# Kernel tuning notes

Hardware: AMD Instinct MI355X
Metric: run time of the kernel (lower is better)

The kernel has to match this reference:

```python
import jax, jax.numpy as jnp
import numpy as np

D = 1024
H = 16
DH = D // H
MAX_TYPES = 256
B, L = 8, 1024
EPS = 1e-5


def setup_inputs() -> dict:
    key = jax.random.key(0)
    ks = jax.random.split(key, 16)
    s = 0.02
    return {
        'type_ids': jax.random.randint(ks[0], (B, L), 0, MAX_TYPES),
        'values': jax.random.normal(ks[1], (B, L, 1), jnp.float32),
        'deltas': jax.random.uniform(ks[2], (B, L, 1), jnp.float32),
        'type_emb': jax.random.normal(ks[3], (MAX_TYPES, D), jnp.float32) * s,
        'Wv': jax.random.normal(ks[4], (D, 1), jnp.float32) * s,
        'bv': jnp.zeros((D,), jnp.float32),
        'Wt': jax.random.normal(ks[5], (D, 1), jnp.float32) * s,
        'bt': jnp.zeros((D,), jnp.float32),
        'Win': jax.random.normal(ks[6], (3 * D, D), jnp.float32) * s,
        'bin': jnp.zeros((3 * D,), jnp.float32),
        'Wout': jax.random.normal(ks[7], (D, D), jnp.float32) * s,
        'bout': jnp.zeros((D,), jnp.float32),
        'W1': jax.random.normal(ks[8], (D, D), jnp.float32) * s,
        'b1': jnp.zeros((D,), jnp.float32),
        'W2': jax.random.normal(ks[9], (D, D), jnp.float32) * s,
        'b2': jnp.zeros((D,), jnp.float32),
        'gamma': jnp.ones((D,), jnp.float32),
        'beta': jnp.zeros((D,), jnp.float32),
    }


def _ln(x, gamma, beta):
    mu = jnp.mean(x, axis=-1, keepdims=True)
    var = jnp.mean(jnp.square(x - mu), axis=-1, keepdims=True)
    return (x - mu) * jax.lax.rsqrt(var + EPS) * gamma + beta


def reference(type_ids, values, deltas, type_emb, Wv, bv, Wt, bt,
              Win, bin, Wout, bout, W1, b1, W2, b2, gamma, beta):
    # fused embedding: type lookup + value/time linear projections
    h = type_emb[type_ids] + values @ Wv.T + bv + deltas @ Wt.T + bt  # [B,L,D]
    b, l, d = h.shape
    # multi-head self-attention (explicit weights path, need_weights=True)
    qkv = h @ Win.T + bin  # [B,L,3D]
    q, k, v = jnp.split(qkv, 3, axis=-1)
    q = q.reshape(b, l, H, DH)
    k = k.reshape(b, l, H, DH)
    v = v.reshape(b, l, H, DH)
    scale = 1.0 / jnp.sqrt(jnp.asarray(DH, h.dtype))
    scores = jnp.einsum('blhd,bmhd->bhlm', q, k) * scale  # [B,H,L,L]
    w = jax.nn.softmax(scores, axis=-1)
    attn = jnp.einsum('bhlm,bmhd->blhd', w, v).reshape(b, l, d)
    attn_out = attn @ Wout.T + bout
    h2 = _ln(h + attn_out, gamma, beta)
    ff = jax.nn.relu(h2 @ W1.T + b1) @ W2.T + b2
    h3 = _ln(h2 + ff, gamma, beta)
    pooled = h3.mean(axis=1)  # [B,D]
    attn_tokens = w.mean(axis=1).mean(axis=2)  # mean over heads, then keys -> [B,L]
    return pooled, attn_tokens
```

## Files before the change

kernel.cpp:

```cpp
#include <hip/hip_runtime.h>
#include <hip/hip_bf16.h>


#define Dm 1024
#define Hh 16
#define Bb 8
#define Ll 1024
#define Mm 8192
#define LNEPS 1e-5f

typedef __attribute__((ext_vector_type(8))) short s16x8;
typedef __attribute__((ext_vector_type(4))) short s16x4;
typedef __attribute__((ext_vector_type(4))) float f32x4;

using bf16 = __hip_bfloat16;

__device__ __forceinline__ short f2bs(float f) {
  return __builtin_bit_cast(short, __float2bfloat16(f));
}
__device__ __forceinline__ float b2f(short s) {
  return __builtin_bit_cast(float, ((unsigned)(unsigned short)s) << 16);
}

__device__ __forceinline__ unsigned cvtpk(float lo, float hi) {
  unsigned r;
  asm("v_cvt_pk_bf16_f32 %0, %1, %2" : "=v"(r) : "v"(lo), "v"(hi));
  return r;
}

__device__ __forceinline__ void gload16(const void* g, void* l) {
  __builtin_amdgcn_global_load_lds(
      (__attribute__((address_space(1))) void*)g,
      (__attribute__((address_space(3))) void*)l, 16, 0, 0);
}

__global__ __launch_bounds__(256) void k_f2b4(
    const float* __restrict__ w0, const float* __restrict__ w1,
    const float* __restrict__ w2, const float* __restrict__ w3,
    bf16* __restrict__ o0, bf16* __restrict__ o1,
    bf16* __restrict__ o2, bf16* __restrict__ o3)
{
  const int bId = blockIdx.x;
  const float* src; bf16* dst; int rel;
  if (bId < 3072)      { src = w0; dst = o0; rel = bId; }
  else if (bId < 4096) { src = w1; dst = o1; rel = bId - 3072; }
  else if (bId < 5120) { src = w2; dst = o2; rel = bId - 4096; }
  else                 { src = w3; dst = o3; rel = bId - 5120; }
  const size_t i = ((size_t)rel * 256 + threadIdx.x) * 4;
  const float4 v = *(const float4*)&src[i];
  s16x4 o;
  o[0] = f2bs(v.x); o[1] = f2bs(v.y); o[2] = f2bs(v.z); o[3] = f2bs(v.w);
  *(s16x4*)&dst[i] = o;
}

__global__ __launch_bounds__(256) void k_embed(
    const int* __restrict__ tids, const float* __restrict__ vals, const float* __restrict__ dels,
    const float* __restrict__ temb, const float* __restrict__ Wv, const float* __restrict__ bv,
    const float* __restrict__ Wt, const float* __restrict__ bt,
    bf16* __restrict__ hb)
{
  const int row = blockIdx.x;
  const int ty = tids[row];
  const float v = vals[row], dl = dels[row];
  const int d0 = threadIdx.x * 4;
  const float4 e  = *(const float4*)&temb[(size_t)ty * Dm + d0];
  const float4 wv = *(const float4*)&Wv[d0];
  const float4 c1 = *(const float4*)&bv[d0];
  const float4 wt = *(const float4*)&Wt[d0];
  const float4 c2 = *(const float4*)&bt[d0];
  s16x4 o;
  o[0] = f2bs(e.x + v * wv.x + c1.x + dl * wt.x + c2.x);
  o[1] = f2bs(e.y + v * wv.y + c1.y + dl * wt.y + c2.y);
  o[2] = f2bs(e.z + v * wv.z + c1.z + dl * wt.z + c2.z);
  o[3] = f2bs(e.w + v * wv.w + c1.w + dl * wt.w + c2.w);
  *(s16x4*)((short*)hb + (size_t)row * Dm + d0) = o;
}

template<bool RELU, bool RES>
__global__ __launch_bounds__(512) void k_gemm8(
    const bf16* __restrict__ A, const bf16* __restrict__ Bt,
    const float* __restrict__ bias, const bf16* __restrict__ res,
    bf16* __restrict__ outB, const int N, const int K)
{
  __shared__ __attribute__((aligned(16))) short lds[49152];
  const int tid = threadIdx.x, lane = tid & 63, wave = tid >> 6;
  const int wr = wave >> 2, wc = wave & 3;
  const int l15 = lane & 15, lg = (lane >> 4) & 3;
  const int bm = blockIdx.x, bn = blockIdx.y;
  const int NT = K >> 6;

  const int rl = tid >> 3;
  const int swz = ((tid & 7) ^ (rl & 7)) * 8;
  const bf16* aSrc = A  + (size_t)(bm * 128 + rl) * K + swz;
  const bf16* bSrc = Bt + (size_t)(bn * 256 + rl) * K + swz;

  f32x4 acc[4][4] = {};

  auto stageA = [&](int t, int h) {
    gload16(aSrc + (size_t)h * 64 * K + t * 64,
            &lds[(t & 1) * 24576 + h * 4096 + tid * 8]);
  };
  auto stageB = [&](int t, int h) {
    gload16(bSrc + (size_t)h * 128 * K + t * 64,
            &lds[(t & 1) * 24576 + 8192 + h * 8192 + tid * 8]);
    gload16(bSrc + (size_t)(h * 128 + 64) * K + t * 64,
            &lds[(t & 1) * 24576 + 8192 + h * 8192 + 4096 + tid * 8]);
  };

  stageA(0, 0); stageA(0, 1); stageB(0, 0); stageB(0, 1);
  if (NT > 1) { stageA(1, 0); stageA(1, 1); }
  asm volatile("s_waitcnt vmcnt(2)" ::: "memory");
  __builtin_amdgcn_sched_barrier(0);
  __builtin_amdgcn_s_barrier();

  for (int t = 0; t < NT; ++t) {
    const int cb = (t & 1) * 24576;
    s16x8 fa[4][2], fb[2][2];

#pragma unroll
    for (int m = 0; m < 4; ++m)
#pragma unroll
      for (int ks = 0; ks < 2; ++ks) {
        const int row = wr * 64 + m * 16 + l15;
        fa[m][ks] = *(const s16x8*)&lds[cb + row * 64 + (((ks * 4 + lg) ^ (row & 7)) << 3)];
      }
#pragma unroll
    for (int n = 0; n < 2; ++n)
#pragma unroll
      for (int ks = 0; ks < 2; ++ks) {
        const int row = wc * 64 + n * 16 + l15;
        fb[n][ks] = *(const s16x8*)&lds[cb + 8192 + row * 64 + (((ks * 4 + lg) ^ (row & 7)) << 3)];
      }
    if (t + 1 < NT) { stageB(t + 1, 0); stageB(t + 1, 1); }
    __builtin_amdgcn_s_barrier();
    asm volatile("s_waitcnt lgkmcnt(0)" ::: "memory");
    __builtin_amdgcn_sched_barrier(0);
    __builtin_amdgcn_s_setprio(1);
#pragma unroll
    for (int m = 0; m < 4; ++m)
#pragma unroll
      for (int n = 0; n < 2; ++n)
#pragma unroll
        for (int ks = 0; ks < 2; ++ks)
          acc[m][n] = __builtin_amdgcn_mfma_f32_16x16x32_bf16(fa[m][ks], fb[n][ks], acc[m][n], 0, 0, 0);
    __builtin_amdgcn_s_setprio(0);
    __builtin_amdgcn_s_barrier();

#pragma unroll
    for (int n = 0; n < 2; ++n)
#pragma unroll
      for (int ks = 0; ks < 2; ++ks) {
        const int row = wc * 64 + (2 + n) * 16 + l15;
        fb[n][ks] = *(const s16x8*)&lds[cb + 8192 + row * 64 + (((ks * 4 + lg) ^ (row & 7)) << 3)];
      }
    if (t + 2 < NT) { stageA(t + 2, 0); stageA(t + 2, 1); }
    __builtin_amdgcn_s_barrier();
    asm volatile("s_waitcnt lgkmcnt(0)" ::: "memory");
    __builtin_amdgcn_sched_barrier(0);
    __builtin_amdgcn_s_setprio(1);
#pragma unroll
    for (int m = 0; m < 4; ++m)
#pragma unroll
      for (int n = 0; n < 2; ++n)
#pragma unroll
        for (int ks = 0; ks < 2; ++ks)
          acc[m][2 + n] = __builtin_amdgcn_mfma_f32_16x16x32_bf16(fa[m][ks], fb[n][ks], acc[m][2 + n], 0, 0, 0);
    __builtin_amdgcn_s_setprio(0);

    if (t + 1 < NT) {
      if (t + 2 < NT) asm volatile("s_waitcnt vmcnt(2)" ::: "memory");
      else            asm volatile("s_waitcnt vmcnt(0)" ::: "memory");
      __builtin_amdgcn_sched_barrier(0);
      __builtin_amdgcn_s_barrier();
    }
  }

#pragma unroll
  for (int n = 0; n < 4; ++n) {
    const int col = bn * 256 + wc * 64 + n * 16 + l15;
    const float bc = bias[col];
#pragma unroll
    for (int m = 0; m < 4; ++m) {
#pragma unroll
      for (int i = 0; i < 4; ++i) {
        const size_t row = (size_t)bm * 128 + wr * 64 + m * 16 + lg * 4 + i;
        float v = acc[m][n][i] + bc;
        if constexpr (RES)  v += b2f(((const short*)res)[row * N + col]);
        if constexpr (RELU) v = fmaxf(v, 0.f);
        outB[row * N + col] = __float2bfloat16(v);
      }
    }
  }
}

__global__ __launch_bounds__(256) void k_vt(const bf16* __restrict__ qkv, bf16* __restrict__ vt)
{
  const int bh = blockIdx.x, lc = blockIdx.y;
  const int b = bh >> 4, h = bh & 15;
  __shared__ short tile[64][72];
  const int r = threadIdx.x >> 2;
  const int c0 = (threadIdx.x & 3) << 4;
  const short* src = (const short*)qkv + ((size_t)(b * Ll + lc * 64 + r)) * 3072 + 2048 + h * 64 + c0;
  const s16x8 x0 = *(const s16x8*)src;
  const s16x8 x1 = *(const s16x8*)(src + 8);
#pragma unroll
  for (int j = 0; j < 8; ++j) { tile[r][c0 + j] = x0[j]; tile[r][c0 + 8 + j] = x1[j]; }
  __syncthreads();
  s16x8 y0, y1;
#pragma unroll
  for (int j = 0; j < 8; ++j) { y0[j] = tile[c0 + j][r]; y1[j] = tile[c0 + 8 + j][r]; }
  short* dst = (short*)vt + ((size_t)(bh * 64 + r)) * Ll + lc * 64 + c0;
  *(s16x8*)dst = y0;
  *(s16x8*)(dst + 8) = y1;
}

__global__ __launch_bounds__(256) void k_attn(
    const bf16* __restrict__ qkv, const bf16* __restrict__ vt, bf16* __restrict__ attnb)
{
  const int bh = blockIdx.x;
  const int qb = blockIdx.y;
  const int b = bh >> 4, h = bh & 15;
  __shared__ __attribute__((aligned(16))) short lK[8192];
  __shared__ __attribute__((aligned(16))) short lV[8192];
  __shared__ __attribute__((aligned(16))) short lP[8192];
  const int tid = threadIdx.x, lane = tid & 63, wave = tid >> 6;
  const int l15 = lane & 15, lg = lane >> 4;
  const int qrow = wave * 32;
  const int l7 = l15 & 7;

  s16x8 qf[2][2];
#pragma unroll
  for (int mq = 0; mq < 2; ++mq)
#pragma unroll
    for (int ks = 0; ks < 2; ++ks)
      qf[mq][ks] = *(const s16x8*)((const short*)qkv +
          ((size_t)(b * Ll + qb * 128 + qrow + mq * 16 + l15)) * 3072 + h * 64 + ks * 32 + lg * 8);

  f32x4 o[2][4] = {};
  float rs[2] = {0.f, 0.f};

  const int sr = tid >> 3;
  const int swz = (tid & 7) ^ (sr & 7);

  auto stage = [&](int mc) {
    const int bo = (mc & 1) * 4096;
    const bf16* gk = qkv + ((size_t)(b * Ll + mc * 64 + sr)) * 3072 + 1024 + h * 64 + swz * 8;
    gload16(gk,                     &lK[bo + tid * 8]);
    gload16(gk + (size_t)32 * 3072, &lK[bo + 2048 + tid * 8]);
    const bf16* gv = vt + ((size_t)(bh * 64 + sr)) * Ll + mc * 64 + swz * 8;
    gload16(gv,                   &lV[bo + tid * 8]);
    gload16(gv + (size_t)32 * Ll, &lV[bo + 2048 + tid * 8]);
  };

  stage(0);

  for (int mc = 0; mc < 16; ++mc) {
    asm volatile("s_waitcnt vmcnt(0)" ::: "memory");
    __builtin_amdgcn_s_barrier();
    __builtin_amdgcn_sched_barrier(0);
    if (mc + 1 < 16) stage(mc + 1);
    const int bo = (mc & 1) * 4096;

    f32x4 st[2][4] = {};
    __builtin_amdgcn_s_setprio(1);
#pragma unroll
    for (int ks = 0; ks < 2; ++ks) {
#pragma unroll
      for (int n = 0; n < 4; ++n) {
        const int kr = n * 16 + l15;
        const s16x8 kf = *(const s16x8*)&lK[bo + kr * 64 + (((ks * 4 + lg) ^ l7) << 3)];
        st[0][n] = __builtin_amdgcn_mfma_f32_16x16x32_bf16(kf, qf[0][ks], st[0][n], 0, 0, 0);
        st[1][n] = __builtin_amdgcn_mfma_f32_16x16x32_bf16(kf, qf[1][ks], st[1][n], 0, 0, 0);
      }
    }
    __builtin_amdgcn_s_setprio(0);

#pragma unroll
    for (int mq = 0; mq < 2; ++mq) {
      const int qr = qrow + mq * 16 + l15;
      short* prow = &lP[qr * 64];
      float loc = 0.f;
#pragma unroll
      for (int n = 0; n < 4; ++n) {
        const float e0 = __expf(st[mq][n][0] * 0.125f);
        const float e1 = __expf(st[mq][n][1] * 0.125f);
        const float e2 = __expf(st[mq][n][2] * 0.125f);
        const float e3 = __expf(st[mq][n][3] * 0.125f);
        loc += (e0 + e1) + (e2 + e3);
        const unsigned c0 = cvtpk(e0, e1);
        const unsigned c1 = cvtpk(e2, e3);
        const int col0 = n * 16 + lg * 4;
        const int scol = ((((col0 >> 3) ^ (qr & 7)) << 3) | (col0 & 7));
        *(unsigned*)&prow[scol]     = c0;
        *(unsigned*)&prow[scol + 2] = c1;
      }
      rs[mq] += loc;
    }

    __builtin_amdgcn_s_setprio(1);
#pragma unroll
    for (int ks = 0; ks < 2; ++ks) {
      s16x8 pa[2];
#pragma unroll
      for (int mq = 0; mq < 2; ++mq) {
        const int qr = qrow + mq * 16 + l15;
        pa[mq] = *(const s16x8*)&lP[qr * 64 + (((ks * 4 + lg) ^ (qr & 7)) << 3)];
      }
#pragma unroll
      for (int dn = 0; dn < 4; ++dn) {
        const int vr = dn * 16 + l15;
        const s16x8 vf = *(const s16x8*)&lV[bo + vr * 64 + (((ks * 4 + lg) ^ l7) << 3)];
        o[0][dn] = __builtin_amdgcn_mfma_f32_16x16x32_bf16(pa[0], vf, o[0][dn], 0, 0, 0);
        o[1][dn] = __builtin_amdgcn_mfma_f32_16x16x32_bf16(pa[1], vf, o[1][dn], 0, 0, 0);
      }
    }
    __builtin_amdgcn_s_setprio(0);
    asm volatile("s_waitcnt lgkmcnt(0)" ::: "memory");
  }

#pragma unroll
  for (int mq = 0; mq < 2; ++mq) {
    rs[mq] += __shfl_xor(rs[mq], 16);
    rs[mq] += __shfl_xor(rs[mq], 32);
  }
#pragma unroll
  for (int mq = 0; mq < 2; ++mq) {
    float inv[4];
#pragma unroll
    for (int i = 0; i < 4; ++i)
      inv[i] = 1.f / __shfl(rs[mq], lg * 4 + i);
#pragma unroll
    for (int dn = 0; dn < 4; ++dn) {
#pragma unroll
      for (int i = 0; i < 4; ++i) {
        const int q = qb * 128 + qrow + mq * 16 + lg * 4 + i;
        attnb[((size_t)(b * Ll + q)) * Dm + h * 64 + dn * 16 + l15] =
            __float2bfloat16(o[mq][dn][i] * inv[i]);
      }
    }
  }
}

__global__ __launch_bounds__(256) void k_ln(const bf16* __restrict__ x,
    const float* __restrict__ gamma, const float* __restrict__ beta,
    bf16* __restrict__ y)
{
  const size_t row = blockIdx.x;
  const int d0 = threadIdx.x * 4;
  const s16x4 xv = *(const s16x4*)((const short*)x + row * Dm + d0);
  float f0 = b2f(xv[0]), f1 = b2f(xv[1]), f2 = b2f(xv[2]), f3 = b2f(xv[3]);
  float s  = (f0 + f1) + (f2 + f3);
  float ss = (f0 * f0 + f1 * f1) + (f2 * f2 + f3 * f3);
#pragma unroll
  for (int m = 1; m < 64; m <<= 1) { s += __shfl_xor(s, m); ss += __shfl_xor(ss, m); }
  __shared__ float red[8];
  const int wv = threadIdx.x >> 6;
  if ((threadIdx.x & 63) == 0) { red[wv] = s; red[4 + wv] = ss; }
  __syncthreads();
  s  = red[0] + red[1] + red[2] + red[3];
  ss = red[4] + red[5] + red[6] + red[7];
  const float mu = s * (1.f / Dm);
  const float rstd = rsqrtf(ss * (1.f / Dm) - mu * mu + LNEPS);
  const float4 g  = *(const float4*)&gamma[d0];
  const float4 be = *(const float4*)&beta[d0];
  s16x4 o;
  o[0] = f2bs((f0 - mu) * rstd * g.x + be.x);
  o[1] = f2bs((f1 - mu) * rstd * g.y + be.y);
  o[2] = f2bs((f2 - mu) * rstd * g.z + be.z);
  o[3] = f2bs((f3 - mu) * rstd * g.w + be.w);
  *(s16x4*)((short*)y + row * Dm + d0) = o;
}

__global__ __launch_bounds__(256) void k_pool_part(const bf16* __restrict__ h3, float* __restrict__ part)
{
  const int b = blockIdx.x, lcn = blockIdx.y, dz = blockIdx.z;
  const int d = dz * 256 + threadIdx.x;
  float s = 0.f;
#pragma unroll 4
  for (int l = 0; l < 64; ++l)
    s += b2f(((const short*)h3)[((size_t)(b * Ll + lcn * 64 + l)) * Dm + d]);
  part[((size_t)(b * 16 + lcn)) * Dm + d] = s;
}

__global__ __launch_bounds__(256) void k_pool_fin(const float* __restrict__ part, float* __restrict__ out)
{
  const int b = blockIdx.x;
  const int d = blockIdx.y * 256 + threadIdx.x;
  float s = 0.f;
#pragma unroll
  for (int c = 0; c < 16; ++c) s += part[((size_t)(b * 16 + c)) * Dm + d];
  out[b * Dm + d] = s * (1.f / Ll);
  out[(size_t)Mm + b * Dm + d] = 1.f / Ll;
}

extern "C" void kernel_launch(void* const* d_in, const int* in_sizes, int n_in,
                              void* d_out, int out_size, void* d_ws, size_t ws_size,
                              hipStream_t stream) {
  const int*   tids  = (const int*)  d_in[0];
  const float* vals  = (const float*)d_in[1];
  const float* dels  = (const float*)d_in[2];
  const float* temb  = (const float*)d_in[3];
  const float* Wv    = (const float*)d_in[4];
  const float* bv    = (const float*)d_in[5];
  const float* Wt    = (const float*)d_in[6];
  const float* bt    = (const float*)d_in[7];
  const float* Win   = (const float*)d_in[8];
  const float* bin   = (const float*)d_in[9];
  const float* Wout  = (const float*)d_in[10];
  const float* bout  = (const float*)d_in[11];
  const float* W1    = (const float*)d_in[12];
  const float* b1    = (const float*)d_in[13];
  const float* W2    = (const float*)d_in[14];
  const float* b2    = (const float*)d_in[15];
  const float* gamma = (const float*)d_in[16];
  const float* beta  = (const float*)d_in[17];
  float* out = (float*)d_out;

  char* w = (char*)d_ws;
  const size_t MB = 1ull << 20;
  bf16*  hb    = (bf16*) (w + 0);
  bf16*  qkv   = (bf16*) (w + 16 * MB);
  bf16*  vtb   = (bf16*) (w + 64 * MB);
  bf16*  attnb = (bf16*) (w + 80 * MB);
  bf16*  x1b   = (bf16*) (w + 16 * MB);
  bf16*  h2b   = (bf16*) (w + 32 * MB);
  bf16*  ff1   = (bf16*) (w + 48 * MB);
  bf16*  x2b   = (bf16*) (w + 64 * MB);
  bf16*  h3b   = (bf16*) (w + 80 * MB);
  bf16*  WinB  = (bf16*) (w + 96 * MB);
  bf16*  WoutB = (bf16*) (w + 102 * MB);
  bf16*  W1B   = (bf16*) (w + 104 * MB);
  bf16*  W2B   = (bf16*) (w + 106 * MB);
  float* part  = (float*)(w + 108 * MB);

  k_f2b4<<<6144, 256, 0, stream>>>(Win, Wout, W1, W2, WinB, WoutB, W1B, W2B);

  k_embed<<<Mm, 256, 0, stream>>>(tids, vals, dels, temb, Wv, bv, Wt, bt, hb);

  k_gemm8<false, false><<<dim3(64, 12), 512, 0, stream>>>(
      hb, WinB, bin, nullptr, qkv, 3072, 1024);

  k_vt<<<dim3(128, 16), 256, 0, stream>>>(qkv, vtb);
  k_attn<<<dim3(128, 8), 256, 0, stream>>>(qkv, vtb, attnb);

  k_gemm8<false, true><<<dim3(64, 4), 512, 0, stream>>>(
      attnb, WoutB, bout, hb, x1b, 1024, 1024);

  k_ln<<<Mm, 256, 0, stream>>>(x1b, gamma, beta, h2b);

  k_gemm8<true, false><<<dim3(64, 4), 512, 0, stream>>>(
      h2b, W1B, b1, nullptr, ff1, 1024, 1024);

  k_gemm8<false, true><<<dim3(64, 4), 512, 0, stream>>>(
      ff1, W2B, b2, h2b, x2b, 1024, 1024);

  k_ln<<<Mm, 256, 0, stream>>>(x2b, gamma, beta, h3b);

  k_pool_part<<<dim3(8, 16, 4), 256, 0, stream>>>(h3b, part);
  k_pool_fin<<<dim3(8, 4), 256, 0, stream>>>(part, out);
}
```

Measured before the change: 242.7 us.

## Use 32x32x16 MFMA in attention and keep P in registers via permlane swap

Rewrites the attention inner loop to use 32x32x16 bf16 MFMAs instead of 16x16x32, and transposes the QK^T accumulator layout in registers with v_permlane32_swap so P feeds the PV MFMA directly. This removes the LDS staging buffer for P, its swizzled stores and reloads, and the trailing lgkmcnt wait. It also switches exp to exp2f with a folded log2e scale. The cost is higher register pressure from the 16-wide accumulators and more complex lane mapping in the normalisation epilogue.

Result: no change. 247.4 us (+1.9%).

```diff
diff --git a/kernel.cpp b/kernel.cpp
--- a/kernel.cpp
+++ b/kernel.cpp
@@ -12,6 +12,7 @@
 typedef __attribute__((ext_vector_type(8))) short s16x8;
 typedef __attribute__((ext_vector_type(4))) short s16x4;
 typedef __attribute__((ext_vector_type(4))) float f32x4;
+typedef __attribute__((ext_vector_type(16))) float f32x16;
 
 using bf16 = __hip_bfloat16;
 
@@ -26,6 +27,9 @@
   unsigned r;
   asm("v_cvt_pk_bf16_f32 %0, %1, %2" : "=v"(r) : "v"(lo), "v"(hi));
   return r;
+}
+__device__ __forceinline__ void perm32(unsigned &a, unsigned &b) {
+  asm volatile("v_permlane32_swap_b32 %0, %1" : "+v"(a), "+v"(b));
 }
 
 __device__ __forceinline__ void gload16(const void* g, void* l) {
@@ -217,27 +221,25 @@
 __global__ __launch_bounds__(256) void k_attn(
     const bf16* __restrict__ qkv, const bf16* __restrict__ vt, bf16* __restrict__ attnb)
 {
-  const int bh = blockIdx.x;
-  const int qb = blockIdx.y;
+  const int bh = blockIdx.x, qb = blockIdx.y;
   const int b = bh >> 4, h = bh & 15;
   __shared__ __attribute__((aligned(16))) short lK[8192];
   __shared__ __attribute__((aligned(16))) short lV[8192];
-  __shared__ __attribute__((aligned(16))) short lP[8192];
   const int tid = threadIdx.x, lane = tid & 63, wave = tid >> 6;
-  const int l15 = lane & 15, lg = lane >> 4;
+  const int l31 = lane & 31, hi = lane >> 5;
+  const int r7 = l31 & 7;
   const int qrow = wave * 32;
-  const int l7 = l15 & 7;
-
-  s16x8 qf[2][2];
-#pragma unroll
-  for (int mq = 0; mq < 2; ++mq)
-#pragma unroll
-    for (int ks = 0; ks < 2; ++ks)
-      qf[mq][ks] = *(const s16x8*)((const short*)qkv +
-          ((size_t)(b * Ll + qb * 128 + qrow + mq * 16 + l15)) * 3072 + h * 64 + ks * 32 + lg * 8);
-
-  f32x4 o[2][4] = {};
-  float rs[2] = {0.f, 0.f};
+
+  s16x8 qf[4];
+  {
+    const short* qp = (const short*)qkv +
+        ((size_t)(b * Ll + qb * 128 + qrow + l31)) * 3072 + h * 64 + hi * 8;
+#pragma unroll
+    for (int s = 0; s < 4; ++s) qf[s] = *(const s16x8*)(qp + s * 16);
+  }
+
+  f32x16 o[2] = {};
+  float rsa[4] = {0.f, 0.f, 0.f, 0.f};
 
   const int sr = tid >> 3;
   const int swz = (tid & 7) ^ (sr & 7);
@@ -245,11 +247,11 @@
   auto stage = [&](int mc) {
     const int bo = (mc & 1) * 4096;
     const bf16* gk = qkv + ((size_t)(b * Ll + mc * 64 + sr)) * 3072 + 1024 + h * 64 + swz * 8;
-    gload16(gk,                     &lK[bo + tid * 8]);
-    gload16(gk + (size_t)32 * 3072, &lK[bo + 2048 + tid * 8]);
+    gload16(gk,                      &lK[bo + tid * 8]);
+    gload16(gk + (size_t)32 * 3072,  &lK[bo + 2048 + tid * 8]);
     const bf16* gv = vt + ((size_t)(bh * 64 + sr)) * Ll + mc * 64 + swz * 8;
-    gload16(gv,                   &lV[bo + tid * 8]);
-    gload16(gv + (size_t)32 * Ll, &lV[bo + 2048 + tid * 8]);
+    gload16(gv,                    &lV[bo + tid * 8]);
+    gload16(gv + (size_t)32 * Ll,  &lV[bo + 2048 + tid * 8]);
   };
 
   stage(0);
@@ -261,82 +263,59 @@
     if (mc + 1 < 16) stage(mc + 1);
     const int bo = (mc & 1) * 4096;
 
-    f32x4 st[2][4] = {};
+    f32x16 st[2] = {};
     __builtin_amdgcn_s_setprio(1);
 #pragma unroll
-    for (int ks = 0; ks < 2; ++ks) {
-#pragma unroll
-      for (int n = 0; n < 4; ++n) {
-        const int kr = n * 16 + l15;
-        const s16x8 kf = *(const s16x8*)&lK[bo + kr * 64 + (((ks * 4 + lg) ^ l7) << 3)];
-        st[0][n] = __builtin_amdgcn_mfma_f32_16x16x32_bf16(kf, qf[0][ks], st[0][n], 0, 0, 0);
-        st[1][n] = __builtin_amdgcn_mfma_f32_16x16x32_bf16(kf, qf[1][ks], st[1][n], 0, 0, 0);
-      }
+    for (int s = 0; s < 4; ++s) {
+      const int sl = ((2 * s + hi) ^ r7) << 3;
+      const s16x8 kf0 = *(const s16x8*)&lK[bo + l31 * 64 + sl];
+      const s16x8 kf1 = *(const s16x8*)&lK[bo + (32 + l31) * 64 + sl];
+      st[0] = __builtin_amdgcn_mfma_f32_32x32x16_bf16(kf0, qf[s], st[0], 0, 0, 0);
+      st[1] = __builtin_amdgcn_mfma_f32_32x32x16_bf16(kf1, qf[s], st[1], 0, 0, 0);
     }
     __builtin_amdgcn_s_setprio(0);
 
 #pragma unroll
-    for (int mq = 0; mq < 2; ++mq) {
-      const int qr = qrow + mq * 16 + l15;
-      short* prow = &lP[qr * 64];
-      float loc = 0.f;
-#pragma unroll
-      for (int n = 0; n < 4; ++n) {
-        const float e0 = __expf(st[mq][n][0] * 0.125f);
-        const float e1 = __expf(st[mq][n][1] * 0.125f);
-        const float e2 = __expf(st[mq][n][2] * 0.125f);
-        const float e3 = __expf(st[mq][n][3] * 0.125f);
-        loc += (e0 + e1) + (e2 + e3);
-        const unsigned c0 = cvtpk(e0, e1);
-        const unsigned c1 = cvtpk(e2, e3);
-        const int col0 = n * 16 + lg * 4;
-        const int scol = ((((col0 >> 3) ^ (qr & 7)) << 3) | (col0 & 7));
-        *(unsigned*)&prow[scol]     = c0;
-        *(unsigned*)&prow[scol + 2] = c1;
-      }
-      rs[mq] += loc;
+    for (int t = 0; t < 2; ++t) {
+#pragma unroll
+      for (int r = 0; r < 16; ++r) {
+        const float e = exp2f(st[t][r] * 0.18033688f);
+        rsa[r & 3] += e;
+        st[t][r] = e;
+      }
+#pragma unroll
+      for (int g = 0; g < 2; ++g) {
+        unsigned c0 = cvtpk(st[t][8 * g + 0], st[t][8 * g + 1]);
+        unsigned c1 = cvtpk(st[t][8 * g + 2], st[t][8 * g + 3]);
+        unsigned c2 = cvtpk(st[t][8 * g + 4], st[t][8 * g + 5]);
+        unsigned c3 = cvtpk(st[t][8 * g + 6], st[t][8 * g + 7]);
+        perm32(c0, c2);
+        perm32(c1, c3);
+        uint4 wda; wda.x = c0; wda.y = c1; wda.z = c2; wda.w = c3;
+        const s16x8 pa = __builtin_bit_cast(s16x8, wda);
+        const int s = 2 * t + g;
+        const int sl = ((2 * s + hi) ^ r7) << 3;
+        const s16x8 vf0 = *(const s16x8*)&lV[bo + l31 * 64 + sl];
+        const s16x8 vf1 = *(const s16x8*)&lV[bo + (32 + l31) * 64 + sl];
+        o[0] = __builtin_amdgcn_mfma_f32_32x32x16_bf16(pa, vf0, o[0], 0, 0, 0);
+        o[1] = __builtin_amdgcn_mfma_f32_32x32x16_bf16(pa, vf1, o[1], 0, 0, 0);
+      }
     }
-
-    __builtin_amdgcn_s_setprio(1);
-#pragma unroll
-    for (int ks = 0; ks < 2; ++ks) {
-      s16x8 pa[2];
-#pragma unroll
-      for (int mq = 0; mq < 2; ++mq) {
-        const int qr = qrow + mq * 16 + l15;
-        pa[mq] = *(const s16x8*)&lP[qr * 64 + (((ks * 4 + lg) ^ (qr & 7)) << 3)];
-      }
-#pragma unroll
-      for (int dn = 0; dn < 4; ++dn) {
-        const int vr = dn * 16 + l15;
-        const s16x8 vf = *(const s16x8*)&lV[bo + vr * 64 + (((ks * 4 + lg) ^ l7) << 3)];
-        o[0][dn] = __builtin_amdgcn_mfma_f32_16x16x32_bf16(pa[0], vf, o[0][dn], 0, 0, 0);
-        o[1][dn] = __builtin_amdgcn_mfma_f32_16x16x32_bf16(pa[1], vf, o[1][dn], 0, 0, 0);
-      }
-    }
-    __builtin_amdgcn_s_setprio(0);
-    asm volatile("s_waitcnt lgkmcnt(0)" ::: "memory");
   }
 
-#pragma unroll
-  for (int mq = 0; mq < 2; ++mq) {
-    rs[mq] += __shfl_xor(rs[mq], 16);
-    rs[mq] += __shfl_xor(rs[mq], 32);
-  }
-#pragma unroll
-  for (int mq = 0; mq < 2; ++mq) {
-    float inv[4];
-#pragma unroll
-    for (int i = 0; i < 4; ++i)
-      inv[i] = 1.f / __shfl(rs[mq], lg * 4 + i);
-#pragma unroll
-    for (int dn = 0; dn < 4; ++dn) {
-#pragma unroll
-      for (int i = 0; i < 4; ++i) {
-        const int q = qb * 128 + qrow + mq * 16 + lg * 4 + i;
-        attnb[((size_t)(b * Ll + q)) * Dm + h * 64 + dn * 16 + l15] =
-            __float2bfloat16(o[mq][dn][i] * inv[i]);
-      }
+  float rs = (rsa[0] + rsa[1]) + (rsa[2] + rsa[3]);
+  rs += __shfl_xor(rs, 32);
+  float inv[16];
+#pragma unroll
+  for (int r = 0; r < 16; ++r)
+    inv[r] = 1.f / __shfl(rs, (r & 3) + 8 * (r >> 2) + 4 * hi);
+#pragma unroll
+  for (int t = 0; t < 2; ++t) {
+#pragma unroll
+    for (int r = 0; r < 16; ++r) {
+      const int q = qb * 128 + qrow + (r & 3) + 8 * (r >> 2) + 4 * hi;
+      attnb[((size_t)(b * Ll + q)) * Dm + h * 64 + t * 32 + l31] =
+          __float2bfloat16(o[t][r] * inv[r]);
     }
   }
 }
```

## Fuse V transpose into QKV GEMM epilogue, fold softmax scale into Wq

Applied to the files above, without the earlier changes.

Merges weight conversion and embedding into a single prep kernel. The QKV GEMM epilogue now writes V directly in transposed per-head layout, replacing the separate transpose kernel. The softmax scale times log2(e) is folded into the Q weights and bias so attention can use exp2 without a multiply. This removes two launches and one pass over V, at the cost of strided, less coalesced 8-byte stores in the GEMM epilogue.

New measurement: 230.0 us, median of 2. -5.3%, faster.

```diff
diff --git a/kernel.cpp b/kernel.cpp
--- a/kernel.cpp
+++ b/kernel.cpp
@@ -8,6 +8,7 @@
 #define Ll 1024
 #define Mm 8192
 #define LNEPS 1e-5f
+#define QSCALE 0.18033688f
 
 typedef __attribute__((ext_vector_type(8))) short s16x8;
 typedef __attribute__((ext_vector_type(4))) short s16x4;
@@ -34,53 +35,54 @@
       (__attribute__((address_space(3))) void*)l, 16, 0, 0);
 }
 
-__global__ __launch_bounds__(256) void k_f2b4(
+__global__ __launch_bounds__(256) void k_prep(
     const float* __restrict__ w0, const float* __restrict__ w1,
     const float* __restrict__ w2, const float* __restrict__ w3,
     bf16* __restrict__ o0, bf16* __restrict__ o1,
-    bf16* __restrict__ o2, bf16* __restrict__ o3)
-{
-  const int bId = blockIdx.x;
-  const float* src; bf16* dst; int rel;
-  if (bId < 3072)      { src = w0; dst = o0; rel = bId; }
-  else if (bId < 4096) { src = w1; dst = o1; rel = bId - 3072; }
-  else if (bId < 5120) { src = w2; dst = o2; rel = bId - 4096; }
-  else                 { src = w3; dst = o3; rel = bId - 5120; }
-  const size_t i = ((size_t)rel * 256 + threadIdx.x) * 4;
-  const float4 v = *(const float4*)&src[i];
-  s16x4 o;
-  o[0] = f2bs(v.x); o[1] = f2bs(v.y); o[2] = f2bs(v.z); o[3] = f2bs(v.w);
-  *(s16x4*)&dst[i] = o;
-}
-
-__global__ __launch_bounds__(256) void k_embed(
-    const int* __restrict__ tids, const float* __restrict__ vals, const float* __restrict__ dels,
-    const float* __restrict__ temb, const float* __restrict__ Wv, const float* __restrict__ bv,
+    bf16* __restrict__ o2, bf16* __restrict__ o3,
+    const int* __restrict__ tids, const float* __restrict__ vals,
+    const float* __restrict__ dels, const float* __restrict__ temb,
+    const float* __restrict__ Wv, const float* __restrict__ bv,
     const float* __restrict__ Wt, const float* __restrict__ bt,
     bf16* __restrict__ hb)
 {
-  const int row = blockIdx.x;
-  const int ty = tids[row];
-  const float v = vals[row], dl = dels[row];
-  const int d0 = threadIdx.x * 4;
-  const float4 e  = *(const float4*)&temb[(size_t)ty * Dm + d0];
-  const float4 wv = *(const float4*)&Wv[d0];
-  const float4 c1 = *(const float4*)&bv[d0];
-  const float4 wt = *(const float4*)&Wt[d0];
-  const float4 c2 = *(const float4*)&bt[d0];
-  s16x4 o;
-  o[0] = f2bs(e.x + v * wv.x + c1.x + dl * wt.x + c2.x);
-  o[1] = f2bs(e.y + v * wv.y + c1.y + dl * wt.y + c2.y);
-  o[2] = f2bs(e.z + v * wv.z + c1.z + dl * wt.z + c2.z);
-  o[3] = f2bs(e.w + v * wv.w + c1.w + dl * wt.w + c2.w);
-  *(s16x4*)((short*)hb + (size_t)row * Dm + d0) = o;
-}
-
-template<bool RELU, bool RES>
+  const int bId = blockIdx.x;
+  if (bId < 6144) {
+    const float* src; bf16* dst; int rel;
+    float sc = 1.f;
+    if (bId < 3072)      { src = w0; dst = o0; rel = bId; if (bId < 1024) sc = QSCALE; }
+    else if (bId < 4096) { src = w1; dst = o1; rel = bId - 3072; }
+    else if (bId < 5120) { src = w2; dst = o2; rel = bId - 4096; }
+    else                 { src = w3; dst = o3; rel = bId - 5120; }
+    const size_t i = ((size_t)rel * 256 + threadIdx.x) * 4;
+    const float4 v = *(const float4*)&src[i];
+    s16x4 o;
+    o[0] = f2bs(v.x * sc); o[1] = f2bs(v.y * sc); o[2] = f2bs(v.z * sc); o[3] = f2bs(v.w * sc);
+    *(s16x4*)&dst[i] = o;
+  } else {
+    const int row = bId - 6144;
+    const int ty = tids[row];
+    const float v = vals[row], dl = dels[row];
+    const int d0 = threadIdx.x * 4;
+    const float4 e  = *(const float4*)&temb[(size_t)ty * Dm + d0];
+    const float4 wv = *(const float4*)&Wv[d0];
+    const float4 c1 = *(const float4*)&bv[d0];
+    const float4 wt = *(const float4*)&Wt[d0];
+    const float4 c2 = *(const float4*)&bt[d0];
+    s16x4 o;
+    o[0] = f2bs(e.x + v * wv.x + c1.x + dl * wt.x + c2.x);
+    o[1] = f2bs(e.y + v * wv.y + c1.y + dl * wt.y + c2.y);
+    o[2] = f2bs(e.z + v * wv.z + c1.z + dl * wt.z + c2.z);
+    o[3] = f2bs(e.w + v * wv.w + c1.w + dl * wt.w + c2.w);
+    *(s16x4*)((short*)hb + (size_t)row * Dm + d0) = o;
+  }
+}
+
+template<bool RELU, bool RES, bool QS, bool VT>
 __global__ __launch_bounds__(512) void k_gemm8(
     const bf16* __restrict__ A, const bf16* __restrict__ Bt,
     const float* __restrict__ bias, const bf16* __restrict__ res,
-    bf16* __restrict__ outB, const int N, const int K)
+    bf16* __restrict__ outB, bf16* __restrict__ vt, const int N, const int K)
 {
   __shared__ __attribute__((aligned(16))) short lds[49152];
   const int tid = threadIdx.x, lane = tid & 63, wave = tid >> 6;
@@ -178,7 +180,23 @@
 #pragma unroll
   for (int n = 0; n < 4; ++n) {
     const int col = bn * 256 + wc * 64 + n * 16 + l15;
-    const float bc = bias[col];
+    float bc = bias[col];
+    if constexpr (QS) { if (col < 1024) bc *= QSCALE; }
+    if constexpr (VT) {
+      if (col >= 2048) {
+        const int hh = (col - 2048) >> 6, dh = (col - 2048) & 63;
+#pragma unroll
+        for (int m = 0; m < 4; ++m) {
+          const size_t row0 = (size_t)bm * 128 + wr * 64 + m * 16 + lg * 4;
+          const int bb = (int)(row0 >> 10), l0 = (int)(row0 & 1023);
+          s16x4 pk;
+#pragma unroll
+          for (int i = 0; i < 4; ++i) pk[i] = f2bs(acc[m][n][i] + bc);
+          *(s16x4*)((short*)vt + ((size_t)((bb * 16 + hh) * 64 + dh)) * Ll + l0) = pk;
+        }
+        continue;
+      }
+    }
 #pragma unroll
     for (int m = 0; m < 4; ++m) {
 #pragma unroll
@@ -191,27 +209,6 @@
       }
     }
   }
-}
-
-__global__ __launch_bounds__(256) void k_vt(const bf16* __restrict__ qkv, bf16* __restrict__ vt)
-{
-  const int bh = blockIdx.x, lc = blockIdx.y;
-  const int b = bh >> 4, h = bh & 15;
-  __shared__ short tile[64][72];
-  const int r = threadIdx.x >> 2;
-  const int c0 = (threadIdx.x & 3) << 4;
-  const short* src = (const short*)qkv + ((size_t)(b * Ll + lc * 64 + r)) * 3072 + 2048 + h * 64 + c0;
-  const s16x8 x0 = *(const s16x8*)src;
-  const s16x8 x1 = *(const s16x8*)(src + 8);
-#pragma unroll
-  for (int j = 0; j < 8; ++j) { tile[r][c0 + j] = x0[j]; tile[r][c0 + 8 + j] = x1[j]; }
-  __syncthreads();
-  s16x8 y0, y1;
-#pragma unroll
-  for (int j = 0; j < 8; ++j) { y0[j] = tile[c0 + j][r]; y1[j] = tile[c0 + 8 + j][r]; }
-  short* dst = (short*)vt + ((size_t)(bh * 64 + r)) * Ll + lc * 64 + c0;
-  *(s16x8*)dst = y0;
-  *(s16x8*)(dst + 8) = y1;
 }
 
 __global__ __launch_bounds__(256) void k_attn(
@@ -282,10 +279,10 @@
       float loc = 0.f;
 #pragma unroll
       for (int n = 0; n < 4; ++n) {
-        const float e0 = __expf(st[mq][n][0] * 0.125f);
-        const float e1 = __expf(st[mq][n][1] * 0.125f);
-        const float e2 = __expf(st[mq][n][2] * 0.125f);
-        const float e3 = __expf(st[mq][n][3] * 0.125f);
+        const float e0 = __builtin_amdgcn_exp2f(st[mq][n][0]);
+        const float e1 = __builtin_amdgcn_exp2f(st[mq][n][1]);
+        const float e2 = __builtin_amdgcn_exp2f(st[mq][n][2]);
+        const float e3 = __builtin_amdgcn_exp2f(st[mq][n][3]);
         loc += (e0 + e1) + (e2 + e3);
         const unsigned c0 = cvtpk(e0, e1);
         const unsigned c1 = cvtpk(e2, e3);
@@ -433,26 +430,24 @@
   bf16*  W2B   = (bf16*) (w + 106 * MB);
   float* part  = (float*)(w + 108 * MB);
 
-  k_f2b4<<<6144, 256, 0, stream>>>(Win, Wout, W1, W2, WinB, WoutB, W1B, W2B);
-
-  k_embed<<<Mm, 256, 0, stream>>>(tids, vals, dels, temb, Wv, bv, Wt, bt, hb);
-
-  k_gemm8<false, false><<<dim3(64, 12), 512, 0, stream>>>(
-      hb, WinB, bin, nullptr, qkv, 3072, 1024);
-
-  k_vt<<<dim3(128, 16), 256, 0, stream>>>(qkv, vtb);
+  k_prep<<<14336, 256, 0, stream>>>(Win, Wout, W1, W2, WinB, WoutB, W1B, W2B,
+                                    tids, vals, dels, temb, Wv, bv, Wt, bt, hb);
+
+  k_gemm8<false, false, true, true><<<dim3(64, 12), 512, 0, stream>>>(
+      hb, WinB, bin, nullptr, qkv, vtb, 3072, 1024);
+
   k_attn<<<dim3(128, 8), 256, 0, stream>>>(qkv, vtb, attnb);
 
-  k_gemm8<false, true><<<dim3(64, 4), 512, 0, stream>>>(
-      attnb, WoutB, bout, hb, x1b, 1024, 1024);
+  k_gemm8<false, true, false, false><<<dim3(64, 4), 512, 0, stream>>>(
+      attnb, WoutB, bout, hb, x1b, nullptr, 1024, 1024);
 
   k_ln<<<Mm, 256, 0, stream>>>(x1b, gamma, beta, h2b);
 
-  k_gemm8<true, false><<<dim3(64, 4), 512, 0, stream>>>(
-      h2b, W1B, b1, nullptr, ff1, 1024, 1024);
-
-  k_gemm8<false, true><<<dim3(64, 4), 512, 0, stream>>>(
-      ff1, W2B, b2, h2b, x2b, 1024, 1024);
+  k_gemm8<true, false, false, false><<<dim3(64, 4), 512, 0, stream>>>(
+      h2b, W1B, b1, nullptr, ff1, nullptr, 1024, 1024);
+
+  k_gemm8<false, true, false, false><<<dim3(64, 4), 512, 0, stream>>>(
+      ff1, W2B, b2, h2b, x2b, nullptr, 1024, 1024);
 
   k_ln<<<Mm, 256, 0, stream>>>(x2b, gamma, beta, h3b);
 
```
